# Performance work log

Hardware: AMD Instinct MI355X
Metric: run time of the kernel (lower is better)

## Reference

```python
import math
import jax, jax.numpy as jnp
import numpy as np

EPS = 1e-6


def setup_inputs() -> dict:
    B, L, D, S, R, H = 4, 1024, 1024, 32, 6, 256
    key = jax.random.key(0)
    ks = jax.random.split(key, 12)
    std = 0.02
    return {
        "x": jax.random.normal(ks[0], (B, L, D), jnp.float32),
        "role_emb": jax.random.normal(ks[1], (S, R, D), jnp.float32) * std,
        "Wr1x": jax.random.normal(ks[2], (S, R, D, H), jnp.float32) * std,
        "Wr1r": jax.random.normal(ks[3], (S, R, D, H), jnp.float32) * std,
        "br1": jnp.zeros((S, R, H), jnp.float32),
        "Wr2": jax.random.normal(ks[4], (S, R, H), jnp.float32) * std,
        "br2": jnp.zeros((S, R), jnp.float32),
        "schema_emb": jax.random.normal(ks[5], (S, D), jnp.float32) * std,
        "Wf1": jax.random.normal(ks[6], (S, D, H), jnp.float32) * std,
        "bf1": jnp.zeros((S, H), jnp.float32),
        "Wf2": jax.random.normal(ks[7], (S, H), jnp.float32) * std,
        "bf2": jnp.zeros((S,), jnp.float32),
        "Wp1": jax.random.normal(ks[8], (R * D, 2 * H), jnp.float32) * std,
        "bp1": jnp.zeros((2 * H,), jnp.float32),
        "Wp2": jax.random.normal(ks[9], (2 * H, D), jnp.float32) * std,
        "bp2": jnp.zeros((D,), jnp.float32),
        "Wsel1": jax.random.normal(ks[10], (D, H), jnp.float32) * std,
        "bsel1": jnp.zeros((H,), jnp.float32),
        "Wsel2": jax.random.normal(ks[11], (H, S), jnp.float32) * std,
        "bsel2": jnp.zeros((S,), jnp.float32),
        "norm_w": jnp.ones((D,), jnp.float32),
    }


def _gelu(x):
    return jax.nn.gelu(x, approximate=False)  # torch nn.GELU default is exact erf


def reference(x, role_emb, Wr1x, Wr1r, br1, Wr2, br2, schema_emb, Wf1, bf1, Wf2,
              bf2, Wp1, bp1, Wp2, bp2, Wsel1, bsel1, Wsel2, bsel2, norm_w):
    B, L, D = x.shape
    S, R, _, H = Wr1x.shape
    n_bind_iters = 3

    # --- per-(schema, role) binding scores (grouped tiny MLPs) ---
    role_bias = jnp.einsum('srd,srdh->srh', role_emb, Wr1r) + br1          # [S,R,H]
    h = jnp.einsum('bld,srdh->bsrlh', x, Wr1x) + role_bias[None, :, :, None, :]
    h = _gelu(h)                                                            # [B,S,R,L,H]
    scores = jax.nn.sigmoid(jnp.einsum('bsrlh,srh->bsrl', h, Wr2)
                            + br2[None, :, :, None])                        # [B,S,R,L]

    # --- iterative softmax binding refinement ---
    inv_sqrt_d = 1.0 / math.sqrt(D)
    for _ in range(n_bind_iters):
        role_probs = jax.nn.softmax(scores, axis=2)        # over roles
        token_probs = jax.nn.softmax(scores * inv_sqrt_d, axis=-1)  # over tokens
        scores = role_probs * token_probs * scores
    filler_weights = jax.nn.softmax(scores, axis=-1)                        # [B,S,R,L]
    bindings = jnp.einsum('bsrl,bld->bsrd', filler_weights, x)              # [B,S,R,D]

    # --- per-schema fit heads ---
    xm = x.mean(axis=1)                                                     # [B,D]
    fit_in = schema_emb[None, :, :] + xm[:, None, :]                        # [B,S,D]
    fh = _gelu(jnp.einsum('bsd,sdh->bsh', fit_in, Wf1) + bf1)
    fit_scores = jax.nn.sigmoid(jnp.einsum('bsh,sh->bs', fh, Wf2) + bf2)    # [B,S]

    # --- schema selection ---
    sel_logits = _gelu(xm @ Wsel1 + bsel1) @ Wsel2 + bsel2                  # [B,S]
    selection_w = jax.nn.softmax(sel_logits + fit_scores, axis=-1)
    best_schema = jnp.argmax(selection_w, axis=-1)                          # [B]

    # --- weighted binding readout + projection ---
    bound_weighted = jnp.einsum('bsrd,bs->brd', bindings, selection_w)      # [B,R,D]
    bound_flat = bound_weighted.reshape(B, R * D)
    schema_repr = _gelu(bound_flat @ Wp1 + bp1) @ Wp2 + bp2                 # [B,D]

    y = x + schema_repr[:, None, :] * 0.1
    x_schema = y * jax.lax.rsqrt(jnp.mean(y * y, axis=-1, keepdims=True) + EPS) * norm_w
    return (x_schema, fit_scores, selection_w, best_schema, bound_weighted)
```

## Files before the change

kernel.cpp:

```cpp
#include <hip/hip_runtime.h>
#include <hip/hip_bf16.h>

#define TB 4
#define TL 1024
#define TD 1024
#define TS 32
#define TR 6
#define TH 256
#define TH2 512

static __device__ __forceinline__ float gelu_f(float v) {
    return 0.5f * v * (1.0f + erff(v * 0.70710678118654752440f));
}

static constexpr float INVL = 1.0f / 1024.0f;

__device__ __align__(16) float g_partxm[TB * 32 * TD];
__device__ __align__(16) float g_fhpart[16 * TB * TS * TH];
__device__ __align__(16) float g_pre1p[192 * TB * TH2];
__device__ __align__(16) float g_selp[TB * 16 * TH];
__device__ __align__(16) float g_srepr[TB * TD];

__global__ void k_xm_part(const float* __restrict__ x) {
    int b = blockIdx.x, lc = blockIdx.y, t = threadIdx.x;
    const float4* xp = (const float4*)(x + ((size_t)b * TL + (size_t)lc * 32) * TD) + t;
    float4 s = {0.f, 0.f, 0.f, 0.f};
    #pragma unroll 8
    for (int i = 0; i < 32; ++i) {
        float4 v = xp[(size_t)i * 256];
        s.x += v.x; s.y += v.y; s.z += v.z; s.w += v.w;
    }
    ((float4*)(g_partxm + ((size_t)b * 32 + lc) * TD))[t] = s;
}

__global__ void __launch_bounds__(1024) k_parts(
        const float* __restrict__ se,  const float* __restrict__ Wf1,
        const float* __restrict__ Wp1, const float* __restrict__ Wsel1,
        float* __restrict__ out_bw) {
    const int bid = blockIdx.x, t = threadIdx.x;
    __shared__ float s_xm[4][256];

    if (bid < 128) {
        const int s = bid >> 2, dc = bid & 3;
        {
            const int b = t >> 8, dq = t & 255, d = dc * 256 + dq;
            float acc = 0.f;
            for (int lc = 0; lc < 32; ++lc) acc += g_partxm[((size_t)b * 32 + lc) * TD + d];
            s_xm[b][dq] = acc * INVL;
        }
        __syncthreads();
        const int h = t & 255, di = t >> 8;
        const int d0 = dc * 256 + di * 64;
        float a0 = 0.f, a1 = 0.f, a2 = 0.f, a3 = 0.f;
        #pragma unroll 4
        for (int i = 0; i < 64; ++i) {
            const int d = d0 + i, dl = di * 64 + i;
            float w = Wf1[((size_t)s * TD + d) * TH + h];
            float sed = se[s * TD + d];
            a0 = fmaf(sed + s_xm[0][dl], w, a0);
            a1 = fmaf(sed + s_xm[1][dl], w, a1);
            a2 = fmaf(sed + s_xm[2][dl], w, a2);
            a3 = fmaf(sed + s_xm[3][dl], w, a3);
        }
        const int part = dc * 4 + di;
        g_fhpart[((size_t)(part * TB + 0) * TS + s) * TH + h] = a0;
        g_fhpart[((size_t)(part * TB + 1) * TS + s) * TH + h] = a1;
        g_fhpart[((size_t)(part * TB + 2) * TS + s) * TH + h] = a2;
        g_fhpart[((size_t)(part * TB + 3) * TS + s) * TH + h] = a3;
    } else if (bid < 224) {
        const int rc = bid - 128;
        if (t < 256) {
            const int b = t >> 6, dq = t & 63, d = (rc & 15) * 64 + dq;
            float acc = 0.f;
            for (int lc = 0; lc < 32; ++lc) acc += g_partxm[((size_t)b * 32 + lc) * TD + d];
            s_xm[b][dq] = acc * INVL;
        }
        __syncthreads();
        const int j = t & 511, ri = t >> 9;
        float a0 = 0.f, a1 = 0.f, a2 = 0.f, a3 = 0.f;
        #pragma unroll 4
        for (int k = 0; k < 32; ++k) {
            const int rowi = rc * 64 + ri * 32 + k;
            const int dl = ri * 32 + k;
            float w = Wp1[(size_t)rowi * TH2 + j];
            a0 = fmaf(s_xm[0][dl], w, a0);
            a1 = fmaf(s_xm[1][dl], w, a1);
            a2 = fmaf(s_xm[2][dl], w, a2);
            a3 = fmaf(s_xm[3][dl], w, a3);
        }
        const int part = rc * 2 + ri;
        g_pre1p[(size_t)(part * TB + 0) * TH2 + j] = a0;
        g_pre1p[(size_t)(part * TB + 1) * TH2 + j] = a1;
        g_pre1p[(size_t)(part * TB + 2) * TH2 + j] = a2;
        g_pre1p[(size_t)(part * TB + 3) * TH2 + j] = a3;
    } else if (bid < 240) {
        const int bi = bid - 224, b = bi >> 2, sl = bi & 3;
        if (t < 256) {
            const int dq = t, d = sl * 256 + dq;
            float acc = 0.f;
            for (int lc = 0; lc < 32; ++lc) acc += g_partxm[((size_t)b * 32 + lc) * TD + d];
            s_xm[0][dq] = acc * INVL;
        }
        __syncthreads();
        const int h = t & 255, q = t >> 8;
        float a0 = 0.f, a1 = 0.f;
        #pragma unroll 4
        for (int i = 0; i < 64; i += 2) {
            const int dl = q * 64 + i, d = sl * 256 + dl;
            a0 = fmaf(s_xm[0][dl],     Wsel1[(size_t)d * TH + h],       a0);
            a1 = fmaf(s_xm[0][dl + 1], Wsel1[(size_t)(d + 1) * TH + h], a1);
        }
        g_selp[(size_t)(b * 16 + sl * 4 + q) * TH + h] = a0 + a1;
    } else {
        const int b = bid - 240;
        float acc = 0.f;
        for (int lc = 0; lc < 32; ++lc) acc += g_partxm[((size_t)b * 32 + lc) * TD + t];
        const float xm = acc * INVL;
        #pragma unroll
        for (int r = 0; r < TR; ++r)
            out_bw[(size_t)(b * TR + r) * TD + t] = xm;
    }
}

__global__ void __launch_bounds__(1024) k_finish(
        const float* __restrict__ bf1,   const float* __restrict__ Wf2,
        const float* __restrict__ bf2v,
        const float* __restrict__ bp1,   const float* __restrict__ Wp2,
        const float* __restrict__ bp2,
        const float* __restrict__ bsel1, const float* __restrict__ Wsel2,
        const float* __restrict__ bsel2,
        float* __restrict__ out_fit, float* __restrict__ out_selw,
        float* __restrict__ out_best) {
    const int bid = blockIdx.x, t = threadIdx.x;
    __shared__ float s_h2[TH2];
    __shared__ float s_pacc[16][64];
    __shared__ float s_sfit[TS];
    __shared__ float s_hs[TH];
    __shared__ float s_sred[8][TS];
    __shared__ float s_lg[TS];

    if (bid < TB) {
        const int b = bid;
        {
            int s = t >> 5, lane = t & 31;
            float v = 0.f;
            #pragma unroll
            for (int k = 0; k < 8; ++k) {
                int h = lane + 32 * k;
                float pre = bf1[s * TH + h];
                #pragma unroll
                for (int p = 0; p < 16; ++p)
                    pre += g_fhpart[((size_t)(p * TB + b) * TS + s) * TH + h];
                v += gelu_f(pre) * Wf2[s * TH + h];
            }
            #pragma unroll
            for (int o = 16; o > 0; o >>= 1) v += __shfl_down(v, o, 32);
            if (lane == 0) {
                float fs = 1.0f / (1.0f + expf(-(v + bf2v[s])));
                s_sfit[s] = fs;
                out_fit[b * TS + s] = fs;
            }
        }
        if (t < TH) {
            float pre = bsel1[t];
            #pragma unroll
            for (int idx = 0; idx < 16; ++idx)
                pre += g_selp[(size_t)(b * 16 + idx) * TH + t];
            s_hs[t] = gelu_f(pre);
        }
        __syncthreads();
        if (t < 256) {
            int s = t & 31, kc = t >> 5;
            float p = 0.f;
            #pragma unroll 4
            for (int k = kc * 32; k < kc * 32 + 32; ++k)
                p = fmaf(s_hs[k], Wsel2[k * TS + s], p);
            s_sred[kc][s] = p;
        }
        __syncthreads();
        if (t < TS) {
            float l = bsel2[t] + s_sfit[t];
            #pragma unroll
            for (int kc = 0; kc < 8; ++kc) l += s_sred[kc][t];
            s_lg[t] = l;
        }
        __syncthreads();
        if (t == 0) {
            float mx = s_lg[0];
            for (int s2 = 1; s2 < TS; ++s2) mx = fmaxf(mx, s_lg[s2]);
            float w[TS];
            float sum = 0.f;
            for (int s2 = 0; s2 < TS; ++s2) { w[s2] = expf(s_lg[s2] - mx); sum += w[s2]; }
            float inv = 1.0f / sum;
            int best = 0; float bwv = -1.f;
            for (int s2 = 0; s2 < TS; ++s2) {
                float wv = w[s2] * inv;
                out_selw[b * TS + s2] = wv;
                if (wv > bwv) { bwv = wv; best = s2; }
            }
            out_best[b] = (float)best;
        }
    } else if (bid < 68) {
        const int g = bid - 4;
        const int b = g >> 4, dc = g & 15;
        if (t < TH2) {
            float p0 = 0.f, p1 = 0.f, p2 = 0.f, p3 = 0.f;
            for (int p = 0; p < 192; p += 4) {
                p0 += g_pre1p[(size_t)((p + 0) * TB + b) * TH2 + t];
                p1 += g_pre1p[(size_t)((p + 1) * TB + b) * TH2 + t];
                p2 += g_pre1p[(size_t)((p + 2) * TB + b) * TH2 + t];
                p3 += g_pre1p[(size_t)((p + 3) * TB + b) * TH2 + t];
            }
            s_h2[t] = gelu_f(bp1[t] + ((p0 + p1) + (p2 + p3)));
        }
        __syncthreads();
        {
            const int dq = t & 63, jh = t >> 6;
            const int d = dc * 64 + dq;
            float acc = 0.f;
            #pragma unroll 4
            for (int j = jh * 32; j < jh * 32 + 32; ++j)
                acc = fmaf(s_h2[j], Wp2[(size_t)j * TD + d], acc);
            s_pacc[jh][dq] = acc;
        }
        __syncthreads();
        if (t < 64) {
            const int d = dc * 64 + t;
            float acc = bp2[d];
            #pragma unroll
            for (int jh = 0; jh < 16; ++jh) acc += s_pacc[jh][t];
            g_srepr[b * TD + d] = acc;
        }
    }
}

__global__ void k_final(const float* __restrict__ x, const float* __restrict__ nw,
                        float* __restrict__ outx) {
    __shared__ float red[4];
    int t = threadIdx.x;
    const float4 nv = ((const float4*)nw)[t];
    #pragma unroll
    for (int rr = 0; rr < 2; ++rr) {
        int row = blockIdx.x * 2 + rr;
        int b = row >> 10;
        const float4 xv = ((const float4*)(x + (size_t)row * TD))[t];
        const float4 sv = ((const float4*)(g_srepr + b * TD))[t];
        float y0 = xv.x + 0.1f * sv.x;
        float y1 = xv.y + 0.1f * sv.y;
        float y2 = xv.z + 0.1f * sv.z;
        float y3 = xv.w + 0.1f * sv.w;
        float ss = y0 * y0 + y1 * y1 + y2 * y2 + y3 * y3;
        #pragma unroll
        for (int o = 32; o > 0; o >>= 1) ss += __shfl_down(ss, o);
        if ((t & 63) == 0) red[t >> 6] = ss;
        __syncthreads();
        float tot = (red[0] + red[1]) + (red[2] + red[3]);
        float sc = rsqrtf(tot * INVL + 1e-6f);
        float4 o4;
        o4.x = y0 * sc * nv.x;
        o4.y = y1 * sc * nv.y;
        o4.z = y2 * sc * nv.z;
        o4.w = y3 * sc * nv.w;
        ((float4*)outx)[(size_t)row * 256 + t] = o4;
        __syncthreads();
    }
}

extern "C" void kernel_launch(void* const* d_in, const int* in_sizes, int n_in,
                              void* d_out, int out_size, void* d_ws, size_t ws_size,
                              hipStream_t stream) {
    const float* x          = (const float*)d_in[0];
    const float* se    = (const float*)d_in[7];
    const float* Wf1   = (const float*)d_in[8];
    const float* bf1   = (const float*)d_in[9];
    const float* Wf2   = (const float*)d_in[10];
    const float* bf2v  = (const float*)d_in[11];
    const float* Wp1   = (const float*)d_in[12];
    const float* bp1   = (const float*)d_in[13];
    const float* Wp2   = (const float*)d_in[14];
    const float* bp2   = (const float*)d_in[15];
    const float* Wsel1 = (const float*)d_in[16];
    const float* bsel1 = (const float*)d_in[17];
    const float* Wsel2 = (const float*)d_in[18];
    const float* bsel2 = (const float*)d_in[19];
    const float* nw    = (const float*)d_in[20];

    float* out      = (float*)d_out;
    float* out_x    = out;
    float* out_fit  = out + 4194304;
    float* out_selw = out + 4194432;
    float* out_best = out + 4194560;
    float* out_bw   = out + 4194564;

    k_xm_part<<<dim3(TB, 32), 256, 0, stream>>>(x);
    k_parts  <<<244,         1024, 0, stream>>>(se, Wf1, Wp1, Wsel1, out_bw);
    k_finish <<<68,          1024, 0, stream>>>(bf1, Wf2, bf2v, bp1, Wp2, bp2,
                                                bsel1, Wsel2, bsel2,
                                                out_fit, out_selw, out_best);
    k_final  <<<TB * TL / 2,  256, 0, stream>>>(x, nw, out_x);
}
```

Measured before the change: 46.80 us.

## Fuse projection head into RMSNorm kernel, recomputing schema_repr per block

Merges the finishing kernel and the final RMSNorm kernel into one launch. Each of 64 blocks recomputes the full per-batch Wp2 projection into shared memory, then normalizes 64 rows of x. This removes a kernel launch and the global round trip for schema_repr. In exchange each block reads all of Wp2 (2 MB per block, 16x redundant per batch), and the memory-bound RMSNorm now runs on only 64 blocks of 512 threads instead of 2048 blocks, which may underfill the GPU.

```diff
diff --git a/kernel.cpp b/kernel.cpp
--- a/kernel.cpp
+++ b/kernel.cpp
@@ -19,7 +19,6 @@
 __device__ __align__(16) float g_fhpart[16 * TB * TS * TH];
 __device__ __align__(16) float g_pre1p[192 * TB * TH2];
 __device__ __align__(16) float g_selp[TB * 16 * TH];
-__device__ __align__(16) float g_srepr[TB * TD];
 
 __global__ void k_xm_part(const float* __restrict__ x) {
     int b = blockIdx.x, lc = blockIdx.y, t = threadIdx.x;
@@ -122,31 +121,30 @@
     }
 }
 
-__global__ void __launch_bounds__(1024) k_finish(
+__global__ void __launch_bounds__(512) k_fin3(
         const float* __restrict__ bf1,   const float* __restrict__ Wf2,
         const float* __restrict__ bf2v,
         const float* __restrict__ bp1,   const float* __restrict__ Wp2,
         const float* __restrict__ bp2,
         const float* __restrict__ bsel1, const float* __restrict__ Wsel2,
         const float* __restrict__ bsel2,
+        const float* __restrict__ x,     const float* __restrict__ nw,
         float* __restrict__ out_fit, float* __restrict__ out_selw,
-        float* __restrict__ out_best) {
+        float* __restrict__ out_best, float* __restrict__ out_x) {
     const int bid = blockIdx.x, t = threadIdx.x;
-    __shared__ float s_h2[TH2];
-    __shared__ float s_pacc[16][64];
-    __shared__ float s_sfit[TS];
-    __shared__ float s_hs[TH];
-    __shared__ float s_sred[8][TS];
-    __shared__ float s_lg[TS];
 
     if (bid < TB) {
+        __shared__ float sfit[TS];
+        __shared__ float hs[TH];
+        __shared__ float sred[256];
+        __shared__ float lg[TS];
         const int b = bid;
         {
-            int s = t >> 5, lane = t & 31;
+            const int s = t >> 4, lane = t & 15;
             float v = 0.f;
             #pragma unroll
-            for (int k = 0; k < 8; ++k) {
-                int h = lane + 32 * k;
+            for (int k = 0; k < 16; ++k) {
+                const int h = lane + 16 * k;
                 float pre = bf1[s * TH + h];
                 #pragma unroll
                 for (int p = 0; p < 16; ++p)
@@ -154,43 +152,44 @@
                 v += gelu_f(pre) * Wf2[s * TH + h];
             }
             #pragma unroll
-            for (int o = 16; o > 0; o >>= 1) v += __shfl_down(v, o, 32);
+            for (int o = 8; o > 0; o >>= 1) v += __shfl_down(v, o, 16);
             if (lane == 0) {
                 float fs = 1.0f / (1.0f + expf(-(v + bf2v[s])));
-                s_sfit[s] = fs;
+                sfit[s] = fs;
                 out_fit[b * TS + s] = fs;
             }
         }
+        __syncthreads();
         if (t < TH) {
             float pre = bsel1[t];
             #pragma unroll
             for (int idx = 0; idx < 16; ++idx)
                 pre += g_selp[(size_t)(b * 16 + idx) * TH + t];
-            s_hs[t] = gelu_f(pre);
+            hs[t] = gelu_f(pre);
         }
         __syncthreads();
         if (t < 256) {
-            int s = t & 31, kc = t >> 5;
+            const int s = t & 31, kc = t >> 5;
             float p = 0.f;
             #pragma unroll 4
             for (int k = kc * 32; k < kc * 32 + 32; ++k)
-                p = fmaf(s_hs[k], Wsel2[k * TS + s], p);
-            s_sred[kc][s] = p;
+                p = fmaf(hs[k], Wsel2[k * TS + s], p);
+            sred[kc * 32 + s] = p;
         }
         __syncthreads();
         if (t < TS) {
-            float l = bsel2[t] + s_sfit[t];
-            #pragma unroll
-            for (int kc = 0; kc < 8; ++kc) l += s_sred[kc][t];
-            s_lg[t] = l;
+            float l = bsel2[t] + sfit[t];
+            #pragma unroll
+            for (int kc = 0; kc < 8; ++kc) l += sred[kc * 32 + t];
+            lg[t] = l;
         }
         __syncthreads();
         if (t == 0) {
-            float mx = s_lg[0];
-            for (int s2 = 1; s2 < TS; ++s2) mx = fmaxf(mx, s_lg[s2]);
+            float mx = lg[0];
+            for (int s2 = 1; s2 < TS; ++s2) mx = fmaxf(mx, lg[s2]);
             float w[TS];
             float sum = 0.f;
-            for (int s2 = 0; s2 < TS; ++s2) { w[s2] = expf(s_lg[s2] - mx); sum += w[s2]; }
+            for (int s2 = 0; s2 < TS; ++s2) { w[s2] = expf(lg[s2] - mx); sum += w[s2]; }
             float inv = 1.0f / sum;
             int best = 0; float bwv = -1.f;
             for (int s2 = 0; s2 < TS; ++s2) {
@@ -200,10 +199,12 @@
             }
             out_best[b] = (float)best;
         }
-    } else if (bid < 68) {
-        const int g = bid - 4;
-        const int b = g >> 4, dc = g & 15;
-        if (t < TH2) {
+    } else {
+        __shared__ float s_h2[TH2];
+        __shared__ float s_sr[TD];
+        __shared__ float red[8];
+        const int i = bid - TB, b = i >> 4, chunk = i & 15;
+        {
             float p0 = 0.f, p1 = 0.f, p2 = 0.f, p3 = 0.f;
             for (int p = 0; p < 192; p += 4) {
                 p0 += g_pre1p[(size_t)((p + 0) * TB + b) * TH2 + t];
@@ -215,54 +216,45 @@
         }
         __syncthreads();
         {
-            const int dq = t & 63, jh = t >> 6;
-            const int d = dc * 64 + dq;
-            float acc = 0.f;
+            float aex = 0.f, aey = 0.f, aox = 0.f, aoy = 0.f;
             #pragma unroll 4
-            for (int j = jh * 32; j < jh * 32 + 32; ++j)
-                acc = fmaf(s_h2[j], Wp2[(size_t)j * TD + d], acc);
-            s_pacc[jh][dq] = acc;
-        }
-        __syncthreads();
-        if (t < 64) {
-            const int d = dc * 64 + t;
-            float acc = bp2[d];
-            #pragma unroll
-            for (int jh = 0; jh < 16; ++jh) acc += s_pacc[jh][t];
-            g_srepr[b * TD + d] = acc;
-        }
-    }
-}
-
-__global__ void k_final(const float* __restrict__ x, const float* __restrict__ nw,
-                        float* __restrict__ outx) {
-    __shared__ float red[4];
-    int t = threadIdx.x;
-    const float4 nv = ((const float4*)nw)[t];
-    #pragma unroll
-    for (int rr = 0; rr < 2; ++rr) {
-        int row = blockIdx.x * 2 + rr;
-        int b = row >> 10;
-        const float4 xv = ((const float4*)(x + (size_t)row * TD))[t];
-        const float4 sv = ((const float4*)(g_srepr + b * TD))[t];
-        float y0 = xv.x + 0.1f * sv.x;
-        float y1 = xv.y + 0.1f * sv.y;
-        float y2 = xv.z + 0.1f * sv.z;
-        float y3 = xv.w + 0.1f * sv.w;
-        float ss = y0 * y0 + y1 * y1 + y2 * y2 + y3 * y3;
-        #pragma unroll
-        for (int o = 32; o > 0; o >>= 1) ss += __shfl_down(ss, o);
-        if ((t & 63) == 0) red[t >> 6] = ss;
-        __syncthreads();
-        float tot = (red[0] + red[1]) + (red[2] + red[3]);
-        float sc = rsqrtf(tot * INVL + 1e-6f);
-        float4 o4;
-        o4.x = y0 * sc * nv.x;
-        o4.y = y1 * sc * nv.y;
-        o4.z = y2 * sc * nv.z;
-        o4.w = y3 * sc * nv.w;
-        ((float4*)outx)[(size_t)row * 256 + t] = o4;
-        __syncthreads();
+            for (int j = 0; j < TH2; j += 2) {
+                const float he = s_h2[j], ho = s_h2[j + 1];
+                const float2 we = *(const float2*)(Wp2 + (size_t)j * TD + 2 * t);
+                const float2 wo = *(const float2*)(Wp2 + (size_t)(j + 1) * TD + 2 * t);
+                aex = fmaf(he, we.x, aex); aey = fmaf(he, we.y, aey);
+                aox = fmaf(ho, wo.x, aox); aoy = fmaf(ho, wo.y, aoy);
+            }
+            s_sr[2 * t]     = (aex + aox) + bp2[2 * t];
+            s_sr[2 * t + 1] = (aey + aoy) + bp2[2 * t + 1];
+        }
+        __syncthreads();
+        const int q = t & 255, r2 = t >> 8, wave = t >> 6;
+        const float4 nv = ((const float4*)nw)[q];
+        const float4 sv = ((const float4*)s_sr)[q];
+        for (int rr = 0; rr < 32; ++rr) {
+            const int row = b * TL + chunk * 64 + rr * 2 + r2;
+            const float4 xv = ((const float4*)x)[(size_t)row * 256 + q];
+            float y0 = xv.x + 0.1f * sv.x;
+            float y1 = xv.y + 0.1f * sv.y;
+            float y2 = xv.z + 0.1f * sv.z;
+            float y3 = xv.w + 0.1f * sv.w;
+            float ss = y0 * y0 + y1 * y1 + y2 * y2 + y3 * y3;
+            #pragma unroll
+            for (int o = 32; o > 0; o >>= 1) ss += __shfl_down(ss, o);
+            if ((t & 63) == 0) red[wave] = ss;
+            __syncthreads();
+            float tot = (red[r2 * 4 + 0] + red[r2 * 4 + 1])
+                      + (red[r2 * 4 + 2] + red[r2 * 4 + 3]);
+            float sc = rsqrtf(tot * INVL + 1e-6f);
+            float4 o4;
+            o4.x = y0 * sc * nv.x;
+            o4.y = y1 * sc * nv.y;
+            o4.z = y2 * sc * nv.z;
+            o4.w = y3 * sc * nv.w;
+            ((float4*)out_x)[(size_t)row * 256 + q] = o4;
+            __syncthreads();
+        }
     }
 }
 
@@ -294,8 +286,7 @@
 
     k_xm_part<<<dim3(TB, 32), 256, 0, stream>>>(x);
     k_parts  <<<244,         1024, 0, stream>>>(se, Wf1, Wp1, Wsel1, out_bw);
-    k_finish <<<68,          1024, 0, stream>>>(bf1, Wf2, bf2v, bp1, Wp2, bp2,
-                                                bsel1, Wsel2, bsel2,
-                                                out_fit, out_selw, out_best);
-    k_final  <<<TB * TL / 2,  256, 0, stream>>>(x, nw, out_x);
-}
+    k_fin3   <<<68,           512, 0, stream>>>(bf1, Wf2, bf2v, bp1, Wp2, bp2,
+                                                bsel1, Wsel2, bsel2, x, nw,
+                                                out_fit, out_selw, out_best, out_x);
+}
```

Result: slower. 89.12 us (+90.4%).
